# Kernel tuning notes

Measured on AMD Instinct MI355X. Metric: run time of the kernel, lower is better.

Reference implementation:

```python
import jax, jax.numpy as jnp
import numpy as np

# Module constants (from init_kwargs / defaults)
CIN, COUT = 128, 64
H, W = 256, 256
X0, X1 = -50.0, 50.0
Y0, Y1 = -50.0, 50.0
Z0, Z1 = -3.0, 5.0
XRES = (X1 - X0) / W
YRES = (Y1 - Y0) / H
EPS = 1e-5


def setup_inputs() -> dict:
    key = jax.random.key(0)
    ks = jax.random.split(key, 24)
    B, N = 4, 100000
    # Points: x,y in [-55,55], z in [-3.5,5.5] so some points fall outside range (tests valid mask)
    xy = jax.random.uniform(ks[0], (B, N, 2), minval=-55.0, maxval=55.0)
    z = jax.random.uniform(ks[1], (B, N, 1), minval=-3.5, maxval=5.5)
    points = jnp.concatenate([xy, z], axis=-1).astype(jnp.float32)
    features = jax.random.normal(ks[2], (B, N, CIN), dtype=jnp.float32)

    def lin(k, fan_in, shape):
        return jax.random.uniform(k, shape, minval=-1.0, maxval=1.0) / np.sqrt(fan_in)

    inp = dict(points=points, features=features)
    # point_mlp: Linear(131,64) -> BN1d(64) -> ReLU -> Linear(64,64)
    inp['w1'] = lin(ks[3], CIN + 3, (CIN + 3, COUT)).astype(jnp.float32)
    inp['b1'] = lin(ks[4], CIN + 3, (COUT,)).astype(jnp.float32)
    inp['bn1_g'] = jax.random.uniform(ks[5], (COUT,), minval=0.5, maxval=1.5)
    inp['bn1_b'] = 0.1 * jax.random.normal(ks[6], (COUT,))
    inp['bn1_m'] = 0.1 * jax.random.normal(ks[7], (COUT,))
    inp['bn1_v'] = jax.random.uniform(ks[8], (COUT,), minval=0.5, maxval=1.5)
    inp['w2'] = lin(ks[9], COUT, (COUT, COUT)).astype(jnp.float32)
    inp['b2'] = lin(ks[10], COUT, (COUT,)).astype(jnp.float32)
    # bev_conv: Conv(64,64,3)+BN2d+ReLU, Conv(64,64,3)+BN2d+ReLU  (OIHW kernels)
    fan = COUT * 9
    inp['cw1'] = lin(ks[11], fan, (COUT, COUT, 3, 3)).astype(jnp.float32)
    inp['cb1'] = lin(ks[12], fan, (COUT,)).astype(jnp.float32)
    inp['cbn1_g'] = jax.random.uniform(ks[13], (COUT,), minval=0.5, maxval=1.5)
    inp['cbn1_b'] = 0.1 * jax.random.normal(ks[14], (COUT,))
    inp['cbn1_m'] = 0.1 * jax.random.normal(ks[15], (COUT,))
    inp['cbn1_v'] = jax.random.uniform(ks[16], (COUT,), minval=0.5, maxval=1.5)
    inp['cw2'] = lin(ks[17], fan, (COUT, COUT, 3, 3)).astype(jnp.float32)
    inp['cb2'] = lin(ks[18], fan, (COUT,)).astype(jnp.float32)
    inp['cbn2_g'] = jax.random.uniform(ks[19], (COUT,), minval=0.5, maxval=1.5)
    inp['cbn2_b'] = 0.1 * jax.random.normal(ks[20], (COUT,))
    inp['cbn2_m'] = 0.1 * jax.random.normal(ks[21], (COUT,))
    inp['cbn2_v'] = jax.random.uniform(ks[22], (COUT,), minval=0.5, maxval=1.5)
    return {k: jnp.asarray(v, jnp.float32) for k, v in inp.items()}


def _bn(x, g, b, m, v, axis):
    shape = [1] * x.ndim
    shape[axis] = -1
    r = lambda a: a.reshape(shape)
    return (x - r(m)) * jax.lax.rsqrt(r(v) + EPS) * r(g) + r(b)


def _conv(x, w, b):
    y = jax.lax.conv_general_dilated(x, w, (1, 1), 'SAME',
                                     dimension_numbers=('NCHW', 'OIHW', 'NCHW'))
    return y + b[None, :, None, None]


def _forward(points, features, w1, b1, bn1_g, bn1_b, bn1_m, bn1_v, w2, b2,
             cw1, cb1, cbn1_g, cbn1_b, cbn1_m, cbn1_v,
             cw2, cb2, cbn2_g, cbn2_b, cbn2_m, cbn2_v):
    B, N, _ = features.shape
    x, y, z = points[..., 0], points[..., 1], points[..., 2]
    valid = ((x >= X0) & (x < X1) & (y >= Y0) & (y < Y1) & (z >= Z0) & (z < Z1))  # (B,N)
    col = jnp.clip(((x - X0) / XRES).astype(jnp.int32), 0, W - 1)
    row = jnp.clip(((y - Y0) / YRES).astype(jnp.int32), 0, H - 1)

    # position encoding (normalized coords)
    pos = jnp.stack([(x - X0) / (X1 - X0), (y - Y0) / (Y1 - Y0), (z - Z0) / (Z1 - Z0)], axis=-1)
    combined = jnp.concatenate([features, pos], axis=-1)  # (B,N,C+3)

    # point MLP (BN in inference mode with running stats)
    h = jnp.einsum('bnc,co->bno', combined, w1) + b1
    h = jax.nn.relu(_bn(h, bn1_g, bn1_b, bn1_m, bn1_v, axis=2))
    h = jnp.einsum('bnc,co->bno', h, w2) + b2  # (B,N,COUT)

    # scatter-max into BEV grid; bev initialized to zeros, so floor at 0
    seg = (jnp.arange(B, dtype=jnp.int32)[:, None] * H + row) * W + col  # (B,N)
    NEG = jnp.float32(-jnp.inf)
    vals = jnp.where(valid[..., None], h, NEG).reshape(B * N, COUT)
    m = jax.ops.segment_max(vals, seg.reshape(-1), num_segments=B * H * W)
    bev = jnp.maximum(m, 0.0).reshape(B, H, W, COUT).transpose(0, 3, 1, 2)  # (B,COUT,H,W)

    # BEV conv stack
    bev = jax.nn.relu(_bn(_conv(bev, cw1, cb1), cbn1_g, cbn1_b, cbn1_m, cbn1_v, axis=1))
    bev = jax.nn.relu(_bn(_conv(bev, cw2, cb2), cbn2_g, cbn2_b, cbn2_m, cbn2_v, axis=1))
    return bev


def reference(points, features, w1, b1, bn1_g, bn1_b, bn1_m, bn1_v, w2, b2,
              cw1, cb1, cbn1_g, cbn1_b, cbn1_m, cbn1_v,
              cw2, cb2, cbn2_g, cbn2_b, cbn2_m, cbn2_v):
    return _forward(points, features, w1, b1, bn1_g, bn1_b, bn1_m, bn1_v, w2, b2,
                    cw1, cb1, cbn1_g, cbn1_b, cbn1_m, cbn1_v,
                    cw2, cb2, cbn2_g, cbn2_b, cbn2_m, cbn2_v)
```

## Files before the change

kernel.cpp:

```cpp
#include <hip/hip_runtime.h>

typedef __attribute__((ext_vector_type(8))) short short8;
typedef __attribute__((ext_vector_type(4))) float floatx4;

static __device__ __forceinline__ unsigned short f2bf(float f) {
    unsigned int u = __float_as_uint(f);
    unsigned int r = (u + 0x7FFFu + ((u >> 16) & 1u)) >> 16;
    return (unsigned short)r;
}

#define BATCH 4
#define NPTS 100000
#define CIN 128
#define COUT 64
#define HH 256
#define WW 256
#define HP 258
#define WP 258

#define OFF_BUF1 0
#define SZ_BUF   (BATCH * HP * WP * COUT * 2)
#define OFF_BUF2 (OFF_BUF1 + SZ_BUF)
#define OFF_WB1  (OFF_BUF2 + SZ_BUF)
#define SZ_WB    (9 * COUT * COUT * 2)
#define OFF_WB2  (OFF_WB1 + SZ_WB)
#define OFF_BIAS1 (OFF_WB2 + SZ_WB)
#define OFF_BIAS2 (OFF_BIAS1 + 256)
#define OFF_W1T  (OFF_BIAS2 + 256)
#define OFF_B1F  (OFF_W1T + 64 * 160 * 2)
#define OFF_W2T  (OFF_B1F + 256)
#define OFF_B2F  (OFF_W2T + 64 * 64 * 2)

__global__ void prep_weights(const float* __restrict__ cw1, const float* __restrict__ cb1,
                             const float* __restrict__ g1, const float* __restrict__ bb1,
                             const float* __restrict__ m1, const float* __restrict__ v1,
                             const float* __restrict__ cw2, const float* __restrict__ cb2,
                             const float* __restrict__ g2, const float* __restrict__ bb2,
                             const float* __restrict__ m2, const float* __restrict__ v2,
                             unsigned short* __restrict__ Wb1, unsigned short* __restrict__ Wb2,
                             float* __restrict__ bias1, float* __restrict__ bias2) {
    int idx = blockIdx.x * 256 + threadIdx.x;
    int l = idx / 36864;
    int r = idx - l * 36864;
    int ci = r & 63;
    int co = (r >> 6) & 63;
    int tap = r >> 12;
    const float* w  = l ? cw2 : cw1;
    const float* g  = l ? g2  : g1;
    const float* v  = l ? v2  : v1;
    float s = g[co] * rsqrtf(v[co] + 1e-5f);
    float wv = w[(co * 64 + ci) * 9 + tap] * s;
    (l ? Wb2 : Wb1)[(tap * 64 + co) * 64 + ci] = f2bf(wv);
    if (tap == 0 && ci == 0) {
        const float* cb = l ? cb2 : cb1;
        const float* bb = l ? bb2 : bb1;
        const float* m  = l ? m2  : m1;
        (l ? bias2 : bias1)[co] = s * (cb[co] - m[co]) + bb[co];
    }
}

__global__ void prep_mlp(const float* __restrict__ w1, const float* __restrict__ b1,
                         const float* __restrict__ g, const float* __restrict__ bb,
                         const float* __restrict__ m, const float* __restrict__ v,
                         const float* __restrict__ w2, const float* __restrict__ b2,
                         unsigned short* __restrict__ w1T, float* __restrict__ b1f,
                         unsigned short* __restrict__ w2T, float* __restrict__ b2f) {
    int idx = blockIdx.x * 256 + threadIdx.x;
    if (idx < 10240) {
        int co = idx / 160, k = idx - co * 160;
        float rs = g[co] * rsqrtf(v[co] + 1e-5f);
        w1T[idx] = f2bf(k < 131 ? w1[k * 64 + co] * rs : 0.f);
        if (k == 0) b1f[co] = (b1[co] - m[co]) * rs + bb[co];
    }
    if (idx < 4096) {
        int co = idx >> 6, k = idx & 63;
        w2T[idx] = f2bf(w2[k * 64 + co]);
        if (k == 0) b2f[co] = b2[co];
    }
}

__global__ void ring_zero(unsigned short* __restrict__ buf1, unsigned short* __restrict__ buf2) {
    int idx = blockIdx.x * 256 + threadIdx.x;
    if (idx >= 2 * 4 * 1028 * 8) return;
    int c8 = idx & 7;
    int rest = idx >> 3;
    int p = rest % 1028;
    int rest2 = rest / 1028;
    int b = rest2 & 3;
    int which = rest2 >> 2;
    int x, y;
    if (p < 258)      { y = 0;   x = p; }
    else if (p < 516) { y = 257; x = p - 258; }
    else if (p < 772) { x = 0;   y = p - 516 + 1; }
    else              { x = 257; y = p - 772 + 1; }
    unsigned short* dst = (which ? buf2 : buf1) + (((b * HP + y) * WP + x) * 64 + c8 * 8);
    uint4 z = {0u, 0u, 0u, 0u};
    *reinterpret_cast<uint4*>(dst) = z;
}

#define K1 160
#define ASTR 168
#define HSTR 72
__global__ __launch_bounds__(256) void mlp_gemm_scatter(
        const float* __restrict__ points, const float* __restrict__ features,
        const unsigned short* __restrict__ w1T, const float* __restrict__ b1f,
        const unsigned short* __restrict__ w2T, const float* __restrict__ b2f,
        float* __restrict__ bev ) {
    __shared__ unsigned short ldsA[128 * ASTR];
    __shared__ int ldsCell[128];

    const int tid = threadIdx.x;
    {
        const int m = tid >> 1, half = tid & 1;
        const long pt = (long)blockIdx.x * 128 + m;
        const float4* fsrc = reinterpret_cast<const float4*>(features + pt * CIN + half * 64);
        unsigned short* arow = &ldsA[m * ASTR + half * 64];
        #pragma unroll
        for (int i = 0; i < 16; ++i) {
            float4 f = fsrc[i];
            ushort4 o;
            o.x = f2bf(f.x); o.y = f2bf(f.y); o.z = f2bf(f.z); o.w = f2bf(f.w);
            *reinterpret_cast<ushort4*>(arow + i * 4) = o;
        }
        if (half) {
            float x = points[pt * 3 + 0];
            float y = points[pt * 3 + 1];
            float z = points[pt * 3 + 2];
            bool valid = (x >= -50.f) & (x < 50.f) & (y >= -50.f) & (y < 50.f) &
                         (z >= -3.f) & (z < 5.f);
            unsigned short tail[32];
            tail[0] = f2bf((x + 50.f) * 0.01f);
            tail[1] = f2bf((y + 50.f) * 0.01f);
            tail[2] = f2bf((z + 3.f) * 0.125f);
            #pragma unroll
            for (int i = 3; i < 32; ++i) tail[i] = 0;
            #pragma unroll
            for (int i = 0; i < 8; ++i)
                *reinterpret_cast<ushort4*>(&ldsA[m * ASTR + 128 + i * 4]) =
                    *reinterpret_cast<ushort4*>(&tail[i * 4]);
            int cell = -1;
            if (valid) {
                int col = (int)((x + 50.f) / 0.390625f); col = min(max(col, 0), 255);
                int row = (int)((y + 50.f) / 0.390625f); row = min(max(row, 0), 255);
                int b = pt >= 300000 ? 3 : (pt >= 200000 ? 2 : (pt >= 100000 ? 1 : 0));
                cell = (b * HH + row) * WW + col;
            }
            ldsCell[m] = cell;
        }
    }
    __syncthreads();

    const int w = tid >> 6, lane = tid & 63, n = lane & 15, q = lane >> 4;

    floatx4 acc[2][4];
    #pragma unroll
    for (int mt = 0; mt < 2; ++mt)
        #pragma unroll
        for (int nt = 0; nt < 4; ++nt) acc[mt][nt] = (floatx4){0.f, 0.f, 0.f, 0.f};

    #pragma unroll
    for (int ks = 0; ks < 5; ++ks) {
        short8 bf[4];
        #pragma unroll
        for (int nt = 0; nt < 4; ++nt)
            bf[nt] = *reinterpret_cast<const short8*>(w1T + (nt * 16 + n) * K1 + ks * 32 + q * 8);
        #pragma unroll
        for (int mt = 0; mt < 2; ++mt) {
            short8 a = *reinterpret_cast<const short8*>(
                &ldsA[(w * 32 + mt * 16 + n) * ASTR + ks * 32 + q * 8]);
            #pragma unroll
            for (int nt = 0; nt < 4; ++nt)
                acc[mt][nt] = __builtin_amdgcn_mfma_f32_16x16x32_bf16(a, bf[nt], acc[mt][nt], 0, 0, 0);
        }
    }

    float bs1[4];
    #pragma unroll
    for (int nt = 0; nt < 4; ++nt) bs1[nt] = b1f[nt * 16 + n];

    __syncthreads();

    #pragma unroll
    for (int mt = 0; mt < 2; ++mt)
        #pragma unroll
        for (int nt = 0; nt < 4; ++nt)
            #pragma unroll
            for (int r = 0; r < 4; ++r) {
                int mm = w * 32 + mt * 16 + q * 4 + r;
                float hv = fmaxf(acc[mt][nt][r] + bs1[nt], 0.f);
                ldsA[mm * HSTR + nt * 16 + n] = f2bf(hv);
            }
    __syncthreads();

    floatx4 acc2[2][4];
    #pragma unroll
    for (int mt = 0; mt < 2; ++mt)
        #pragma unroll
        for (int nt = 0; nt < 4; ++nt) acc2[mt][nt] = (floatx4){0.f, 0.f, 0.f, 0.f};

    #pragma unroll
    for (int ks = 0; ks < 2; ++ks) {
        short8 bf[4];
        #pragma unroll
        for (int nt = 0; nt < 4; ++nt)
            bf[nt] = *reinterpret_cast<const short8*>(w2T + (nt * 16 + n) * 64 + ks * 32 + q * 8);
        #pragma unroll
        for (int mt = 0; mt < 2; ++mt) {
            short8 a = *reinterpret_cast<const short8*>(
                &ldsA[(w * 32 + mt * 16 + n) * HSTR + ks * 32 + q * 8]);
            #pragma unroll
            for (int nt = 0; nt < 4; ++nt)
                acc2[mt][nt] = __builtin_amdgcn_mfma_f32_16x16x32_bf16(a, bf[nt], acc2[mt][nt], 0, 0, 0);
        }
    }

    float bs2[4];
    #pragma unroll
    for (int nt = 0; nt < 4; ++nt) bs2[nt] = b2f[nt * 16 + n];

    #pragma unroll
    for (int mt = 0; mt < 2; ++mt)
        #pragma unroll
        for (int r = 0; r < 4; ++r) {
            int mm = w * 32 + mt * 16 + q * 4 + r;
            int cell = ldsCell[mm];
            if (cell >= 0) {
                int* base = (int*)bev + cell * 64;
                #pragma unroll
                for (int nt = 0; nt < 4; ++nt) {
                    float val = fmaxf(acc2[mt][nt][r] + bs2[nt], 0.f);
                    atomicMax(base + nt * 16 + n, __float_as_int(val));
                }
            }
        }
}

__global__ __launch_bounds__(256) void bev_to_bf16(const float* __restrict__ bev,
                                                   unsigned short* __restrict__ dst) {
    int idx = blockIdx.x * 256 + threadIdx.x;
    int e = idx * 4;
    int ci = e & 63;
    int pix = e >> 6;
    int xw = pix & 255;
    int rest = pix >> 8;
    int yw = rest & 255;
    int b = rest >> 8;
    const float4 v = *reinterpret_cast<const float4*>(bev + e);
    ushort4 o;
    o.x = f2bf(v.x); o.y = f2bf(v.y); o.z = f2bf(v.z); o.w = f2bf(v.w);
    int pidx = ((b * HP + yw + 1) * WP + xw + 1) * 64 + ci;
    *reinterpret_cast<ushort4*>(dst + pidx) = o;
}

#define PSTR 72
template <bool FINAL>
__global__ __launch_bounds__(256) void conv3x3(const unsigned short* __restrict__ Xp,
                                               const unsigned short* __restrict__ Wb,
                                               const float* __restrict__ bias,
                                               void* __restrict__ out) {
    __shared__ unsigned short lds[3 * 66 * PSTR];

    const int bx = blockIdx.x;
    const int by = blockIdx.y;
    const int bz = blockIdx.z;
    const int tid = threadIdx.x;
    const int x0 = bx * 64;

    for (int ch = tid; ch < 1584; ch += 256) {
        int flat = ch * 8;
        int r = flat / 4224;
        int rem = flat - r * 4224;
        int p = rem >> 6;
        int ci = rem & 63;
        const uint4 v = *reinterpret_cast<const uint4*>(
            Xp + (((bz * HP + by + r) * WP) + x0 + p) * 64 + ci);
        *reinterpret_cast<uint4*>(&lds[(r * 66 + p) * PSTR + ci]) = v;
    }

    const int wv = tid >> 6;
    const int lane = tid & 63;
    const int n = lane & 15;
    const int q = lane >> 4;

    short8 bfrag[9][2];
    #pragma unroll
    for (int t = 0; t < 9; ++t)
        #pragma unroll
        for (int kk = 0; kk < 2; ++kk)
            bfrag[t][kk] = *reinterpret_cast<const short8*>(
                Wb + ((t * 64 + wv * 16 + n) * 64 + kk * 32 + q * 8));

    __syncthreads();

    floatx4 acc[4];
    #pragma unroll
    for (int mt = 0; mt < 4; ++mt) acc[mt] = (floatx4){0.f, 0.f, 0.f, 0.f};

    #pragma unroll
    for (int t = 0; t < 9; ++t) {
        const int dy = t / 3, dx = t % 3;
        const int rowbase = dy * 66 * PSTR;
        #pragma unroll
        for (int kk = 0; kk < 2; ++kk) {
            const int cio = kk * 32 + q * 8;
            #pragma unroll
            for (int mt = 0; mt < 4; ++mt) {
                const int p = mt * 16 + n + dx;
                short8 a = *reinterpret_cast<const short8*>(&lds[rowbase + p * PSTR + cio]);
                acc[mt] = __builtin_amdgcn_mfma_f32_16x16x32_bf16(a, bfrag[t][kk], acc[mt], 0, 0, 0);
            }
        }
    }

    const int co = wv * 16 + n;
    const float bs = bias[co];
    #pragma unroll
    for (int mt = 0; mt < 4; ++mt) {
        #pragma unroll
        for (int r = 0; r < 4; ++r) {
            int px = mt * 16 + q * 4 + r;
            float val = fmaxf(acc[mt][r] + bs, 0.f);
            if (FINAL) {
                ((float*)out)[((bz * 64 + co) * HH + by) * WW + x0 + px] = val;
            } else {
                ((unsigned short*)out)[((bz * HP + by + 1) * WP + (x0 + px + 1)) * 64 + co] = f2bf(val);
            }
        }
    }
}

extern "C" void kernel_launch(void* const* d_in, const int* in_sizes, int n_in,
                              void* d_out, int out_size, void* d_ws, size_t ws_size,
                              hipStream_t stream) {
    const float* points   = (const float*)d_in[0];
    const float* features = (const float*)d_in[1];
    const float* w1   = (const float*)d_in[2];
    const float* b1   = (const float*)d_in[3];
    const float* bn1g = (const float*)d_in[4];
    const float* bn1b = (const float*)d_in[5];
    const float* bn1m = (const float*)d_in[6];
    const float* bn1v = (const float*)d_in[7];
    const float* w2   = (const float*)d_in[8];
    const float* b2   = (const float*)d_in[9];
    const float* cw1  = (const float*)d_in[10];
    const float* cb1  = (const float*)d_in[11];
    const float* cg1  = (const float*)d_in[12];
    const float* cbb1 = (const float*)d_in[13];
    const float* cm1  = (const float*)d_in[14];
    const float* cv1  = (const float*)d_in[15];
    const float* cw2  = (const float*)d_in[16];
    const float* cb2  = (const float*)d_in[17];
    const float* cg2  = (const float*)d_in[18];
    const float* cbb2 = (const float*)d_in[19];
    const float* cm2  = (const float*)d_in[20];
    const float* cv2  = (const float*)d_in[21];

    float* out = (float*)d_out;
    char* ws = (char*)d_ws;
    unsigned short* buf1 = (unsigned short*)(ws + OFF_BUF1);
    unsigned short* buf2 = (unsigned short*)(ws + OFF_BUF2);
    unsigned short* Wb1  = (unsigned short*)(ws + OFF_WB1);
    unsigned short* Wb2  = (unsigned short*)(ws + OFF_WB2);
    float* bias1 = (float*)(ws + OFF_BIAS1);
    float* bias2 = (float*)(ws + OFF_BIAS2);
    unsigned short* w1T = (unsigned short*)(ws + OFF_W1T);
    float* b1f = (float*)(ws + OFF_B1F);
    unsigned short* w2T = (unsigned short*)(ws + OFF_W2T);
    float* b2f = (float*)(ws + OFF_B2F);

    hipMemsetAsync(d_out, 0, (size_t)BATCH * HH * WW * COUT * 4, stream);
    ring_zero<<<(2 * 4 * 1028 * 8 + 255) / 256, 256, 0, stream>>>(buf1, buf2);

    prep_weights<<<288, 256, 0, stream>>>(cw1, cb1, cg1, cbb1, cm1, cv1,
                                          cw2, cb2, cg2, cbb2, cm2, cv2,
                                          Wb1, Wb2, bias1, bias2);
    prep_mlp<<<40, 256, 0, stream>>>(w1, b1, bn1g, bn1b, bn1m, bn1v, w2, b2,
                                     w1T, b1f, w2T, b2f);

    mlp_gemm_scatter<<<(BATCH * NPTS) / 128, 256, 0, stream>>>(
        points, features, w1T, b1f, w2T, b2f, out);

    bev_to_bf16<<<(BATCH * HH * WW * COUT / 4) / 256, 256, 0, stream>>>(out, buf1);

    dim3 cgrid(WW / 64, HH, BATCH);
    conv3x3<false><<<cgrid, 256, 0, stream>>>(buf1, Wb1, bias1, (void*)buf2);
    conv3x3<true><<<cgrid, 256, 0, stream>>>(buf2, Wb2, bias2, (void*)out);
}
```

Baseline: 504.2 us.

## Fuse bf16 conversion into conv load and stream features directly into MFMA

Removes the separate bev_to_bf16 kernel and the padded buf1: the first conv now reads the fp32 scatter grid directly, converts it to bf16 on the fly, and zero-fills the border itself. The MLP kernel no longer stages features in LDS. It loads and converts them straight from global memory into MFMA operands. The three positional inputs are applied as an fp32 rank-3 correction in the epilogue, which shrinks K from 160 to 128. This saves a full read and write pass over the BEV grid and LDS traffic. In exchange, the conv loads twice as many fp32 bytes per tile and feature loads are strided per lane.

```diff
diff --git a/kernel.cpp b/kernel.cpp
--- a/kernel.cpp
+++ b/kernel.cpp
@@ -1,4 +1,5 @@
 #include <hip/hip_runtime.h>
+#include <hip/hip_bf16.h>
 
 typedef __attribute__((ext_vector_type(8))) short short8;
 typedef __attribute__((ext_vector_type(4))) float floatx4;
@@ -7,6 +8,27 @@
     unsigned int u = __float_as_uint(f);
     unsigned int r = (u + 0x7FFFu + ((u >> 16) & 1u)) >> 16;
     return (unsigned short)r;
+}
+
+static __device__ __forceinline__ short8 cvt8(const float* __restrict__ p) {
+    const float4 f0 = *reinterpret_cast<const float4*>(p);
+    const float4 f1 = *reinterpret_cast<const float4*>(p + 4);
+    union { short8 s; __hip_bfloat162 h[4]; } u;
+    u.h[0] = __float22bfloat162_rn(make_float2(f0.x, f0.y));
+    u.h[1] = __float22bfloat162_rn(make_float2(f0.z, f0.w));
+    u.h[2] = __float22bfloat162_rn(make_float2(f1.x, f1.y));
+    u.h[3] = __float22bfloat162_rn(make_float2(f1.z, f1.w));
+    return u.s;
+}
+static __device__ __forceinline__ uint4 cvt8u(const float* __restrict__ p) {
+    const float4 f0 = *reinterpret_cast<const float4*>(p);
+    const float4 f1 = *reinterpret_cast<const float4*>(p + 4);
+    union { uint4 u; __hip_bfloat162 h[4]; } w;
+    w.h[0] = __float22bfloat162_rn(make_float2(f0.x, f0.y));
+    w.h[1] = __float22bfloat162_rn(make_float2(f0.z, f0.w));
+    w.h[2] = __float22bfloat162_rn(make_float2(f1.x, f1.y));
+    w.h[3] = __float22bfloat162_rn(make_float2(f1.z, f1.w));
+    return w.u;
 }
 
 #define BATCH 4
@@ -18,16 +40,16 @@
 #define HP 258
 #define WP 258
 
-#define OFF_BUF1 0
+#define OFF_BUF2 0
 #define SZ_BUF   (BATCH * HP * WP * COUT * 2)
-#define OFF_BUF2 (OFF_BUF1 + SZ_BUF)
 #define OFF_WB1  (OFF_BUF2 + SZ_BUF)
 #define SZ_WB    (9 * COUT * COUT * 2)
 #define OFF_WB2  (OFF_WB1 + SZ_WB)
 #define OFF_BIAS1 (OFF_WB2 + SZ_WB)
 #define OFF_BIAS2 (OFF_BIAS1 + 256)
 #define OFF_W1T  (OFF_BIAS2 + 256)
-#define OFF_B1F  (OFF_W1T + 64 * 160 * 2)
+#define OFF_W1POS (OFF_W1T + 64 * 128 * 2)
+#define OFF_B1F  (OFF_W1POS + 768)
 #define OFF_W2T  (OFF_B1F + 256)
 #define OFF_B2F  (OFF_W2T + 64 * 64 * 2)
 
@@ -63,13 +85,15 @@
                          const float* __restrict__ g, const float* __restrict__ bb,
                          const float* __restrict__ m, const float* __restrict__ v,
                          const float* __restrict__ w2, const float* __restrict__ b2,
-                         unsigned short* __restrict__ w1T, float* __restrict__ b1f,
+                         unsigned short* __restrict__ w1T, float* __restrict__ w1pos,
+                         float* __restrict__ b1f,
                          unsigned short* __restrict__ w2T, float* __restrict__ b2f) {
     int idx = blockIdx.x * 256 + threadIdx.x;
-    if (idx < 10240) {
-        int co = idx / 160, k = idx - co * 160;
+    if (idx < 8192) {
+        int co = idx >> 7, k = idx & 127;
         float rs = g[co] * rsqrtf(v[co] + 1e-5f);
-        w1T[idx] = f2bf(k < 131 ? w1[k * 64 + co] * rs : 0.f);
+        w1T[idx] = f2bf(w1[k * 64 + co] * rs);
+        if (k < 3) w1pos[k * 64 + co] = w1[(128 + k) * 64 + co] * rs;
         if (k == 0) b1f[co] = (b1[co] - m[co]) * rs + bb[co];
     }
     if (idx < 4096) {
@@ -79,78 +103,61 @@
     }
 }
 
-__global__ void ring_zero(unsigned short* __restrict__ buf1, unsigned short* __restrict__ buf2) {
+__global__ void ring_zero(unsigned short* __restrict__ buf2) {
     int idx = blockIdx.x * 256 + threadIdx.x;
-    if (idx >= 2 * 4 * 1028 * 8) return;
+    if (idx >= 4 * 1028 * 8) return;
     int c8 = idx & 7;
     int rest = idx >> 3;
     int p = rest % 1028;
-    int rest2 = rest / 1028;
-    int b = rest2 & 3;
-    int which = rest2 >> 2;
+    int b = rest / 1028;
     int x, y;
     if (p < 258)      { y = 0;   x = p; }
     else if (p < 516) { y = 257; x = p - 258; }
     else if (p < 772) { x = 0;   y = p - 516 + 1; }
     else              { x = 257; y = p - 772 + 1; }
-    unsigned short* dst = (which ? buf2 : buf1) + (((b * HP + y) * WP + x) * 64 + c8 * 8);
+    unsigned short* dst = buf2 + (((b * HP + y) * WP + x) * 64 + c8 * 8);
     uint4 z = {0u, 0u, 0u, 0u};
     *reinterpret_cast<uint4*>(dst) = z;
 }
 
-#define K1 160
-#define ASTR 168
 #define HSTR 72
 __global__ __launch_bounds__(256) void mlp_gemm_scatter(
         const float* __restrict__ points, const float* __restrict__ features,
-        const unsigned short* __restrict__ w1T, const float* __restrict__ b1f,
+        const unsigned short* __restrict__ w1T, const float* __restrict__ w1pos,
+        const float* __restrict__ b1f,
         const unsigned short* __restrict__ w2T, const float* __restrict__ b2f,
         float* __restrict__ bev ) {
-    __shared__ unsigned short ldsA[128 * ASTR];
-    __shared__ int ldsCell[128];
+    __shared__ unsigned short ldsH[128 * HSTR];
+    __shared__ float4 ldsPos[128];
 
     const int tid = threadIdx.x;
-    {
-        const int m = tid >> 1, half = tid & 1;
-        const long pt = (long)blockIdx.x * 128 + m;
-        const float4* fsrc = reinterpret_cast<const float4*>(features + pt * CIN + half * 64);
-        unsigned short* arow = &ldsA[m * ASTR + half * 64];
-        #pragma unroll
-        for (int i = 0; i < 16; ++i) {
-            float4 f = fsrc[i];
-            ushort4 o;
-            o.x = f2bf(f.x); o.y = f2bf(f.y); o.z = f2bf(f.z); o.w = f2bf(f.w);
-            *reinterpret_cast<ushort4*>(arow + i * 4) = o;
-        }
-        if (half) {
-            float x = points[pt * 3 + 0];
-            float y = points[pt * 3 + 1];
-            float z = points[pt * 3 + 2];
-            bool valid = (x >= -50.f) & (x < 50.f) & (y >= -50.f) & (y < 50.f) &
-                         (z >= -3.f) & (z < 5.f);
-            unsigned short tail[32];
-            tail[0] = f2bf((x + 50.f) * 0.01f);
-            tail[1] = f2bf((y + 50.f) * 0.01f);
-            tail[2] = f2bf((z + 3.f) * 0.125f);
-            #pragma unroll
-            for (int i = 3; i < 32; ++i) tail[i] = 0;
-            #pragma unroll
-            for (int i = 0; i < 8; ++i)
-                *reinterpret_cast<ushort4*>(&ldsA[m * ASTR + 128 + i * 4]) =
-                    *reinterpret_cast<ushort4*>(&tail[i * 4]);
-            int cell = -1;
-            if (valid) {
-                int col = (int)((x + 50.f) / 0.390625f); col = min(max(col, 0), 255);
-                int row = (int)((y + 50.f) / 0.390625f); row = min(max(row, 0), 255);
-                int b = pt >= 300000 ? 3 : (pt >= 200000 ? 2 : (pt >= 100000 ? 1 : 0));
-                cell = (b * HH + row) * WW + col;
-            }
-            ldsCell[m] = cell;
-        }
+    const long pt0 = (long)blockIdx.x * 128;
+
+    if (tid < 128) {
+        const long pt = pt0 + tid;
+        const float x = points[pt * 3 + 0];
+        const float y = points[pt * 3 + 1];
+        const float z = points[pt * 3 + 2];
+        const bool valid = (x >= -50.f) & (x < 50.f) & (y >= -50.f) & (y < 50.f) &
+                           (z >= -3.f) & (z < 5.f);
+        int cell = -1;
+        if (valid) {
+            int col = (int)((x + 50.f) / 0.390625f); col = min(max(col, 0), 255);
+            int row = (int)((y + 50.f) / 0.390625f); row = min(max(row, 0), 255);
+            int b = pt >= 300000 ? 3 : (pt >= 200000 ? 2 : (pt >= 100000 ? 1 : 0));
+            cell = (b * HH + row) * WW + col;
+        }
+        float4 v;
+        v.x = (x + 50.f) * 0.01f;
+        v.y = (y + 50.f) * 0.01f;
+        v.z = (z + 3.f) * 0.125f;
+        v.w = __int_as_float(cell);
+        ldsPos[tid] = v;
     }
     __syncthreads();
 
     const int w = tid >> 6, lane = tid & 63, n = lane & 15, q = lane >> 4;
+    const int m0 = w * 32;
 
     floatx4 acc[2][4];
     #pragma unroll
@@ -159,37 +166,41 @@
         for (int nt = 0; nt < 4; ++nt) acc[mt][nt] = (floatx4){0.f, 0.f, 0.f, 0.f};
 
     #pragma unroll
-    for (int ks = 0; ks < 5; ++ks) {
+    for (int ks = 0; ks < 4; ++ks) {
         short8 bf[4];
         #pragma unroll
         for (int nt = 0; nt < 4; ++nt)
-            bf[nt] = *reinterpret_cast<const short8*>(w1T + (nt * 16 + n) * K1 + ks * 32 + q * 8);
+            bf[nt] = *reinterpret_cast<const short8*>(w1T + (nt * 16 + n) * 128 + ks * 32 + q * 8);
         #pragma unroll
         for (int mt = 0; mt < 2; ++mt) {
-            short8 a = *reinterpret_cast<const short8*>(
-                &ldsA[(w * 32 + mt * 16 + n) * ASTR + ks * 32 + q * 8]);
+            short8 a = cvt8(features + (pt0 + m0 + mt * 16 + n) * CIN + ks * 32 + q * 8);
             #pragma unroll
             for (int nt = 0; nt < 4; ++nt)
                 acc[mt][nt] = __builtin_amdgcn_mfma_f32_16x16x32_bf16(a, bf[nt], acc[mt][nt], 0, 0, 0);
         }
     }
 
-    float bs1[4];
-    #pragma unroll
-    for (int nt = 0; nt < 4; ++nt) bs1[nt] = b1f[nt * 16 + n];
-
-    __syncthreads();
+    float w1p[3][4], bs1[4];
+    #pragma unroll
+    for (int nt = 0; nt < 4; ++nt) {
+        bs1[nt] = b1f[nt * 16 + n];
+        #pragma unroll
+        for (int j = 0; j < 3; ++j) w1p[j][nt] = w1pos[j * 64 + nt * 16 + n];
+    }
 
     #pragma unroll
     for (int mt = 0; mt < 2; ++mt)
         #pragma unroll
-        for (int nt = 0; nt < 4; ++nt)
+        for (int r = 0; r < 4; ++r) {
+            const int mm = m0 + mt * 16 + q * 4 + r;
+            const float4 pos = ldsPos[mm];
             #pragma unroll
-            for (int r = 0; r < 4; ++r) {
-                int mm = w * 32 + mt * 16 + q * 4 + r;
-                float hv = fmaxf(acc[mt][nt][r] + bs1[nt], 0.f);
-                ldsA[mm * HSTR + nt * 16 + n] = f2bf(hv);
-            }
+            for (int nt = 0; nt < 4; ++nt) {
+                float hv = acc[mt][nt][r] + bs1[nt]
+                         + pos.x * w1p[0][nt] + pos.y * w1p[1][nt] + pos.z * w1p[2][nt];
+                ldsH[mm * HSTR + nt * 16 + n] = f2bf(fmaxf(hv, 0.f));
+            }
+        }
     __syncthreads();
 
     floatx4 acc2[2][4];
@@ -207,7 +218,7 @@
         #pragma unroll
         for (int mt = 0; mt < 2; ++mt) {
             short8 a = *reinterpret_cast<const short8*>(
-                &ldsA[(w * 32 + mt * 16 + n) * HSTR + ks * 32 + q * 8]);
+                &ldsH[(m0 + mt * 16 + n) * HSTR + ks * 32 + q * 8]);
             #pragma unroll
             for (int nt = 0; nt < 4; ++nt)
                 acc2[mt][nt] = __builtin_amdgcn_mfma_f32_16x16x32_bf16(a, bf[nt], acc2[mt][nt], 0, 0, 0);
@@ -222,10 +233,10 @@
     for (int mt = 0; mt < 2; ++mt)
         #pragma unroll
         for (int r = 0; r < 4; ++r) {
-            int mm = w * 32 + mt * 16 + q * 4 + r;
-            int cell = ldsCell[mm];
+            const int mm = m0 + mt * 16 + q * 4 + r;
+            const int cell = __float_as_int(ldsPos[mm].w);
             if (cell >= 0) {
-                int* base = (int*)bev + cell * 64;
+                int* base = (int*)bev + (long)cell * 64;
                 #pragma unroll
                 for (int nt = 0; nt < 4; ++nt) {
                     float val = fmaxf(acc2[mt][nt][r] + bs2[nt], 0.f);
@@ -235,26 +246,9 @@
         }
 }
 
-__global__ __launch_bounds__(256) void bev_to_bf16(const float* __restrict__ bev,
-                                                   unsigned short* __restrict__ dst) {
-    int idx = blockIdx.x * 256 + threadIdx.x;
-    int e = idx * 4;
-    int ci = e & 63;
-    int pix = e >> 6;
-    int xw = pix & 255;
-    int rest = pix >> 8;
-    int yw = rest & 255;
-    int b = rest >> 8;
-    const float4 v = *reinterpret_cast<const float4*>(bev + e);
-    ushort4 o;
-    o.x = f2bf(v.x); o.y = f2bf(v.y); o.z = f2bf(v.z); o.w = f2bf(v.w);
-    int pidx = ((b * HP + yw + 1) * WP + xw + 1) * 64 + ci;
-    *reinterpret_cast<ushort4*>(dst + pidx) = o;
-}
-
 #define PSTR 72
-template <bool FINAL>
-__global__ __launch_bounds__(256) void conv3x3(const unsigned short* __restrict__ Xp,
+template <bool FINAL, bool SRCF32>
+__global__ __launch_bounds__(256) void conv3x3(const void* __restrict__ Xsrc,
                                                const unsigned short* __restrict__ Wb,
                                                const float* __restrict__ bias,
                                                void* __restrict__ out) {
@@ -272,8 +266,19 @@
         int rem = flat - r * 4224;
         int p = rem >> 6;
         int ci = rem & 63;
-        const uint4 v = *reinterpret_cast<const uint4*>(
-            Xp + (((bz * HP + by + r) * WP) + x0 + p) * 64 + ci);
+        uint4 v;
+        if (SRCF32) {
+            int gy = by + r - 1;
+            int gx = x0 + p - 1;
+            if (gy >= 0 && gy < HH && gx >= 0 && gx < WW) {
+                v = cvt8u((const float*)Xsrc + (((bz * HH + gy) * WW) + gx) * 64 + ci);
+            } else {
+                v = (uint4){0u, 0u, 0u, 0u};
+            }
+        } else {
+            v = *reinterpret_cast<const uint4*>(
+                (const unsigned short*)Xsrc + (((bz * HP + by + r) * WP) + x0 + p) * 64 + ci);
+        }
         *reinterpret_cast<uint4*>(&lds[(r * 66 + p) * PSTR + ci]) = v;
     }
 
@@ -357,32 +362,30 @@
 
     float* out = (float*)d_out;
     char* ws = (char*)d_ws;
-    unsigned short* buf1 = (unsigned short*)(ws + OFF_BUF1);
     unsigned short* buf2 = (unsigned short*)(ws + OFF_BUF2);
     unsigned short* Wb1  = (unsigned short*)(ws + OFF_WB1);
     unsigned short* Wb2  = (unsigned short*)(ws + OFF_WB2);
     float* bias1 = (float*)(ws + OFF_BIAS1);
     float* bias2 = (float*)(ws + OFF_BIAS2);
     unsigned short* w1T = (unsigned short*)(ws + OFF_W1T);
+    float* w1pos = (float*)(ws + OFF_W1POS);
     float* b1f = (float*)(ws + OFF_B1F);
     unsigned short* w2T = (unsigned short*)(ws + OFF_W2T);
     float* b2f = (float*)(ws + OFF_B2F);
 
     hipMemsetAsync(d_out, 0, (size_t)BATCH * HH * WW * COUT * 4, stream);
-    ring_zero<<<(2 * 4 * 1028 * 8 + 255) / 256, 256, 0, stream>>>(buf1, buf2);
+    ring_zero<<<(4 * 1028 * 8 + 255) / 256, 256, 0, stream>>>(buf2);
 
     prep_weights<<<288, 256, 0, stream>>>(cw1, cb1, cg1, cbb1, cm1, cv1,
                                           cw2, cb2, cg2, cbb2, cm2, cv2,
                                           Wb1, Wb2, bias1, bias2);
-    prep_mlp<<<40, 256, 0, stream>>>(w1, b1, bn1g, bn1b, bn1m, bn1v, w2, b2,
-                                     w1T, b1f, w2T, b2f);
+    prep_mlp<<<32, 256, 0, stream>>>(w1, b1, bn1g, bn1b, bn1m, bn1v, w2, b2,
+                                     w1T, w1pos, b1f, w2T, b2f);
 
     mlp_gemm_scatter<<<(BATCH * NPTS) / 128, 256, 0, stream>>>(
-        points, features, w1T, b1f, w2T, b2f, out);
-
-    bev_to_bf16<<<(BATCH * HH * WW * COUT / 4) / 256, 256, 0, stream>>>(out, buf1);
+        points, features, w1T, w1pos, b1f, w2T, b2f, out);
 
     dim3 cgrid(WW / 64, HH, BATCH);
-    conv3x3<false><<<cgrid, 256, 0, stream>>>(buf1, Wb1, bias1, (void*)buf2);
-    conv3x3<true><<<cgrid, 256, 0, stream>>>(buf2, Wb2, bias2, (void*)out);
-}
+    conv3x3<false, true><<<cgrid, 256, 0, stream>>>((const void*)out, Wb1, bias1, (void*)buf2);
+    conv3x3<true, false><<<cgrid, 256, 0, stream>>>((const void*)buf2, Wb2, bias2, (void*)out);
+}
```

Measured after the change: 498.0 us. No clear change (-1.2%).
